# Kernel tuning notes

Hardware: AMD Instinct MI355X
Metric: run time of the kernel (lower is better)

Reference implementation:

```python
import jax, jax.numpy as jnp
import numpy as np

N, E = 50000, 800000
IN_DIM, OUT_DIM, EDGE_DIM = 128, 128, 6
LN_EPS = 1e-5


def setup_inputs() -> dict:
    key = jax.random.key(0)
    ks = jax.random.split(key, 9)
    w = lambda k, sh: (jax.random.normal(k, sh, jnp.float32) * 0.05)
    return {
        "x": jax.random.normal(ks[0], (N, IN_DIM), jnp.float32),
        "edge_attr": jax.random.normal(ks[1], (E, EDGE_DIM), jnp.float32),
        "Wn": w(ks[2], (IN_DIM, OUT_DIM)),
        "bn": jnp.zeros((OUT_DIM,), jnp.float32),
        "We": w(ks[3], (EDGE_DIM, OUT_DIM)),
        "be": jnp.zeros((OUT_DIM,), jnp.float32),
        "Wm": w(ks[4], (2 * OUT_DIM, OUT_DIM)),
        "bm": jnp.zeros((OUT_DIM,), jnp.float32),
        "gamma": jnp.ones((OUT_DIM,), jnp.float32),
        "beta": jnp.zeros((OUT_DIM,), jnp.float32),
        "edge_index": jax.random.randint(ks[5], (2, E), 0, N, jnp.int32),
    }


def reference(x, edge_attr, Wn, bn, We, be, Wm, bm, gamma, beta, edge_index):
    row, col = edge_index[0], edge_index[1]
    x_t = x @ Wn + bn                                  # [N, D]
    e_t = edge_attr @ We + be                          # [E, D]
    msgs = jnp.concatenate([x_t[col], e_t], axis=-1)   # gather + concat [E, 2D]
    msgs = jax.nn.relu(msgs @ Wm + bm)                 # [E, D]
    agg = jax.ops.segment_sum(msgs, row, num_segments=N)            # scatter_add
    deg = jax.ops.segment_sum(jnp.ones((E,), jnp.float32), row, num_segments=N)
    out = agg / jnp.clip(deg, 1.0)[:, None] + x_t      # mean-normalize + residual
    mu = out.mean(axis=-1, keepdims=True)
    var = out.var(axis=-1, keepdims=True)
    return (out - mu) * jax.lax.rsqrt(var + LN_EPS) * gamma + beta
```

## Files before the change

kernel.cpp:

```cpp
#include <hip/hip_runtime.h>
#include <hip/hip_bf16.h>

#define D 128
#define EDGE_DIM 6
#define LN_EPS 1e-5f
#define HIST_BLOCKS 2048

typedef __attribute__((ext_vector_type(8))) short short8;
typedef __attribute__((ext_vector_type(4))) float f32x4;

static __device__ __forceinline__ float bf_lo(unsigned u) { return __uint_as_float(u << 16); }
static __device__ __forceinline__ float bf_hi(unsigned u) { return __uint_as_float(u & 0xffff0000u); }
static __device__ __forceinline__ unsigned short f2bf(float f) {
    __hip_bfloat16 h = __float2bfloat16(f);
    return *reinterpret_cast<unsigned short*>(&h);
}

__global__ __launch_bounds__(128)
void setup_all(const float* __restrict__ Wn, const float* __restrict__ bn,
               const float* __restrict__ We, const float* __restrict__ be,
               const float* __restrict__ Wm, const float* __restrict__ bm,
               const int* __restrict__ ei, int E,
               float* __restrict__ Wnm, float* __restrict__ bnm,
               float* __restrict__ Wc, float* __restrict__ bc,
               int* __restrict__ cnt) {
    const int b = blockIdx.x;
    const int d = threadIdx.x;
    if (b < 128) {
        float acc = 0.f;
#pragma unroll 8
        for (int j = 0; j < D; ++j)
            acc = fmaf(Wn[b * D + j], Wm[j * D + d], acc);
        Wnm[b * D + d] = acc;
    } else if (b == 128) {
        float acc = 0.f;
#pragma unroll 8
        for (int j = 0; j < D; ++j)
            acc = fmaf(bn[j], Wm[j * D + d], acc);
        bnm[d] = acc;
    } else if (b < 135) {
        const int k = b - 129;
        float acc = 0.f;
#pragma unroll 8
        for (int j = 0; j < D; ++j)
            acc = fmaf(We[k * D + j], Wm[(D + j) * D + d], acc);
        Wc[k * D + d] = acc;
    } else if (b == 135) {
        float acc = bm[d];
#pragma unroll 8
        for (int j = 0; j < D; ++j)
            acc = fmaf(be[j], Wm[(D + j) * D + d], acc);
        bc[d] = acc;
    } else {
        for (int i = (b - 136) * 128 + d; i < E; i += HIST_BLOCKS * 128)
            atomicAdd(&cnt[ei[i]], 1);
    }
}

__global__ __launch_bounds__(256)
void pack_wb(const float* __restrict__ Wn, const float* __restrict__ Wnm,
             unsigned short* __restrict__ Wb) {
    const int idx = blockIdx.x * 256 + threadIdx.x;
    if (idx >= 4096) return;
    const int lane = idx & 63;
    const int s = (idx >> 6) & 3;
    const int ct = (idx >> 8) & 7;
    const int mat = idx >> 11;
    const float* W = mat ? Wnm : Wn;
    const int col = ct * 16 + (lane & 15);
    const int k0 = (lane >> 4) * 8 + 32 * s;
    short8 v;
#pragma unroll
    for (int j = 0; j < 8; ++j)
        v[j] = (short)f2bf(W[(size_t)(k0 + j) * D + col]);
    *reinterpret_cast<short8*>(Wb + (size_t)idx * 8) = v;
}

__global__ __launch_bounds__(256)
void gemm_mfma(const float* __restrict__ x, const unsigned short* __restrict__ Wb,
               const float* __restrict__ bn, const float* __restrict__ bnm,
               unsigned short* __restrict__ xtb, unsigned short* __restrict__ hb,
               int nrows) {
    const int lane = threadIdx.x & 63;
    const int wid = threadIdx.x >> 6;
    const int row16 = lane & 15;
    const int kgrp = lane >> 4;
    const int ntile = (nrows + 15) / 16;

    float biasA[8], biasB[8];
#pragma unroll
    for (int ct = 0; ct < 8; ++ct) {
        biasA[ct] = bn[ct * 16 + row16];
        biasB[ct] = bnm[ct * 16 + row16];
    }

    for (int t = blockIdx.x * 4 + wid; t < ntile; t += gridDim.x * 4) {
        const int ra = t * 16 + row16;
        const bool rv = ra < nrows;
        short8 a[4];
#pragma unroll
        for (int s = 0; s < 4; ++s) {
            const float* xp = x + (size_t)ra * D + kgrp * 8 + 32 * s;
            float4 u0 = rv ? *reinterpret_cast<const float4*>(xp)
                           : make_float4(0.f, 0.f, 0.f, 0.f);
            float4 u1 = rv ? *reinterpret_cast<const float4*>(xp + 4)
                           : make_float4(0.f, 0.f, 0.f, 0.f);
            a[s][0] = (short)f2bf(u0.x); a[s][1] = (short)f2bf(u0.y);
            a[s][2] = (short)f2bf(u0.z); a[s][3] = (short)f2bf(u0.w);
            a[s][4] = (short)f2bf(u1.x); a[s][5] = (short)f2bf(u1.y);
            a[s][6] = (short)f2bf(u1.z); a[s][7] = (short)f2bf(u1.w);
        }
        const int rw0 = t * 16 + kgrp * 4;
#pragma unroll
        for (int mat = 0; mat < 2; ++mat) {
            unsigned short* out = mat ? hb : xtb;
#pragma unroll
            for (int ct = 0; ct < 8; ++ct) {
                f32x4 acc = {0.f, 0.f, 0.f, 0.f};
#pragma unroll
                for (int s = 0; s < 4; ++s) {
                    short8 bfr = *reinterpret_cast<const short8*>(
                        Wb + (size_t)((((mat * 8 + ct) * 4 + s) * 64 + lane)) * 8);
                    acc = __builtin_amdgcn_mfma_f32_16x16x32_bf16(a[s], bfr, acc, 0, 0, 0);
                }
                const float bsc = mat ? biasB[ct] : biasA[ct];
                const int dcol = ct * 16 + row16;
#pragma unroll
                for (int j = 0; j < 4; ++j) {
                    const int r = rw0 + j;
                    if (r < nrows) out[(size_t)r * D + dcol] = f2bf(acc[j] + bsc);
                }
            }
        }
    }
}

__global__ __launch_bounds__(1024)
void scan_block_atomic(const int* __restrict__ cnt, int* __restrict__ start,
                       int* __restrict__ cur, int* __restrict__ cursor, int n) {
    __shared__ int wsum[16];
    __shared__ int sbase;
    const int tid = threadIdx.x, lane = tid & 63, wid = tid >> 6;
    const int i = blockIdx.x * 1024 + tid;
    const int v = (i < n) ? cnt[i] : 0;
    int x = v;
#pragma unroll
    for (int off = 1; off < 64; off <<= 1) {
        int t = __shfl_up(x, off);
        if (lane >= off) x += t;
    }
    if (lane == 63) wsum[wid] = x;
    __syncthreads();
    if (wid == 0) {
        int w = (lane < 16) ? wsum[lane] : 0;
#pragma unroll
        for (int off = 1; off < 16; off <<= 1) {
            int t = __shfl_up(w, off);
            if (lane >= off) w += t;
        }
        if (lane < 16) wsum[lane] = w;
    }
    __syncthreads();
    const int total = wsum[15];
    if (tid == 0) sbase = atomicAdd(cursor, total);
    __syncthreads();
    const int woff = (wid > 0) ? wsum[wid - 1] : 0;
    if (i < n) {
        const int sv = sbase + woff + x - v;
        start[i] = sv;
        cur[i] = sv;
    }
}

__global__ void scatter_rec(const int* __restrict__ ei, int E, const float* __restrict__ ea,
                            int* __restrict__ cur, uint4* __restrict__ rec) {
    int e = blockIdx.x * blockDim.x + threadIdx.x;
    if (e < E) {
        int row = ei[e];
        int col = ei[E + e];
        const float* ep = ea + (size_t)e * EDGE_DIM;
        unsigned b01 = (unsigned)f2bf(ep[0]) | ((unsigned)f2bf(ep[1]) << 16);
        unsigned b23 = (unsigned)f2bf(ep[2]) | ((unsigned)f2bf(ep[3]) << 16);
        unsigned b45 = (unsigned)f2bf(ep[4]) | ((unsigned)f2bf(ep[5]) << 16);
        int pos = atomicAdd(&cur[row], 1);
        rec[pos] = make_uint4((unsigned)col, b01, b23, b45);
    }
}

__global__ __launch_bounds__(256)
void aggregate_ln(const unsigned* __restrict__ h,
                  const int* __restrict__ start, const int* __restrict__ cnt,
                  const uint4* __restrict__ rec,
                  const float* __restrict__ Wc, const float* __restrict__ bc,
                  const unsigned* __restrict__ xtb,
                  const float* __restrict__ gamma, const float* __restrict__ beta,
                  float* __restrict__ out, int nnode) {
    const int lane = threadIdx.x & 63;
    const int wid = threadIdx.x >> 6;

    float2 wc[EDGE_DIM];
#pragma unroll
    for (int k = 0; k < EDGE_DIM; ++k)
        wc[k] = reinterpret_cast<const float2*>(Wc)[k * 64 + lane];
    const float2 bc2 = reinterpret_cast<const float2*>(bc)[lane];
    const float2 g = reinterpret_cast<const float2*>(gamma)[lane];
    const float2 bb = reinterpret_cast<const float2*>(beta)[lane];

    for (int n = blockIdx.x * 4 + wid; n < nnode; n += gridDim.x * 4) {
        const int s = start[n];
        const int c = cnt[n];
        float ax = 0.f, ay = 0.f;
        for (int ibase = 0; ibase < c; ibase += 64) {
            const int m = min(64, c - ibase);
            uint4 rc = make_uint4(0, 0, 0, 0);
            if (lane < m) rc = rec[(size_t)(s + ibase) + lane];
            auto LDH = [&](int j) -> unsigned {
                const int jc = min(j, m - 1);
                const int colj = __builtin_amdgcn_readlane((int)rc.x, jc);
                return h[(unsigned)(colj * 64 + lane)];
            };
            auto COMP = [&](int j, unsigned hv) {
                const unsigned b01 = (unsigned)__builtin_amdgcn_readlane((int)rc.y, j);
                const unsigned b23 = (unsigned)__builtin_amdgcn_readlane((int)rc.z, j);
                const unsigned b45 = (unsigned)__builtin_amdgcn_readlane((int)rc.w, j);
                const float e0 = bf_lo(b01), e1 = bf_hi(b01);
                const float e2 = bf_lo(b23), e3 = bf_hi(b23);
                const float e4 = bf_lo(b45), e5 = bf_hi(b45);
                float vx = bc2.x + bf_lo(hv);
                float vy = bc2.y + bf_hi(hv);
                vx = fmaf(e0, wc[0].x, vx); vy = fmaf(e0, wc[0].y, vy);
                vx = fmaf(e1, wc[1].x, vx); vy = fmaf(e1, wc[1].y, vy);
                vx = fmaf(e2, wc[2].x, vx); vy = fmaf(e2, wc[2].y, vy);
                vx = fmaf(e3, wc[3].x, vx); vy = fmaf(e3, wc[3].y, vy);
                vx = fmaf(e4, wc[4].x, vx); vy = fmaf(e4, wc[4].y, vy);
                vx = fmaf(e5, wc[5].x, vx); vy = fmaf(e5, wc[5].y, vy);
                ax += fmaxf(vx, 0.f);
                ay += fmaxf(vy, 0.f);
            };
            unsigned h0 = LDH(0), h1 = LDH(1), h2 = LDH(2), h3 = LDH(3),
                     h4 = LDH(4), h5 = LDH(5), h6 = LDH(6), h7 = LDH(7);
            int i = 0;
            for (; i + 8 <= m; i += 8) {
                COMP(i + 0, h0); h0 = LDH(i + 8);
                COMP(i + 1, h1); h1 = LDH(i + 9);
                COMP(i + 2, h2); h2 = LDH(i + 10);
                COMP(i + 3, h3); h3 = LDH(i + 11);
                COMP(i + 4, h4); h4 = LDH(i + 12);
                COMP(i + 5, h5); h5 = LDH(i + 13);
                COMP(i + 6, h6); h6 = LDH(i + 14);
                COMP(i + 7, h7); h7 = LDH(i + 15);
            }
            if (i + 0 < m) COMP(i + 0, h0);
            if (i + 1 < m) COMP(i + 1, h1);
            if (i + 2 < m) COMP(i + 2, h2);
            if (i + 3 < m) COMP(i + 3, h3);
            if (i + 4 < m) COMP(i + 4, h4);
            if (i + 5 < m) COMP(i + 5, h5);
            if (i + 6 < m) COMP(i + 6, h6);
        }
        const float inv = 1.0f / fmaxf((float)c, 1.0f);
        const unsigned xu = xtb[(unsigned)(n * 64 + lane)];
        float o0 = fmaf(ax, inv, bf_lo(xu));
        float o1 = fmaf(ay, inv, bf_hi(xu));
        float s1 = o0 + o1, s2 = o0 * o0 + o1 * o1;
#pragma unroll
        for (int off = 32; off; off >>= 1) {
            s1 += __shfl_xor(s1, off);
            s2 += __shfl_xor(s2, off);
        }
        const float mean = s1 * (1.0f / D);
        const float var = s2 * (1.0f / D) - mean * mean;
        const float rstd = rsqrtf(var + LN_EPS);
        float2 r;
        r.x = (o0 - mean) * rstd * g.x + bb.x;
        r.y = (o1 - mean) * rstd * g.y + bb.y;
        reinterpret_cast<float2*>(out)[(size_t)n * 64 + lane] = r;
    }
}

extern "C" void kernel_launch(void* const* d_in, const int* in_sizes, int n_in,
                              void* d_out, int out_size, void* d_ws, size_t ws_size,
                              hipStream_t stream) {
    const float* x     = (const float*)d_in[0];
    const float* eattr = (const float*)d_in[1];
    const float* Wn    = (const float*)d_in[2];
    const float* bn    = (const float*)d_in[3];
    const float* We    = (const float*)d_in[4];
    const float* be    = (const float*)d_in[5];
    const float* Wm    = (const float*)d_in[6];
    const float* bm    = (const float*)d_in[7];
    const float* gamma = (const float*)d_in[8];
    const float* beta  = (const float*)d_in[9];
    const int*   ei    = (const int*)d_in[10];

    const int N = in_sizes[0] / D;
    const int E = in_sizes[10] / 2;

    char* ws = (char*)d_ws;
    unsigned short* xtb = (unsigned short*)ws; ws += (size_t)N * D * 2;
    unsigned short* hb  = (unsigned short*)ws; ws += (size_t)N * D * 2;
    int* ints = (int*)ws;                      ws += (size_t)(N + 4) * 4;
    int* cnt = ints;
    int* cursor = ints + N;
    int* cur    = (int*)ws;                    ws += (size_t)N * 4;
    int* startv = (int*)ws;                    ws += (size_t)N * 4;
    uint4* rec  = (uint4*)ws;                  ws += (size_t)E * 16;
    float* Wnm  = (float*)ws;                  ws += (size_t)D * D * 4;
    float* bnm  = (float*)ws;                  ws += (size_t)D * 4;
    float* Wc   = (float*)ws;                  ws += (size_t)EDGE_DIM * D * 4;
    float* bcv  = (float*)ws;                  ws += (size_t)D * 4;
    unsigned short* Wb = (unsigned short*)ws;  ws += (size_t)2 * 8 * 4 * 64 * 8 * 2;

    hipMemsetAsync(ints, 0, (size_t)(N + 4) * 4, stream);

    setup_all<<<136 + HIST_BLOCKS, 128, 0, stream>>>(Wn, bn, We, be, Wm, bm, ei, E,
                                                     Wnm, bnm, Wc, bcv, cnt);
    pack_wb<<<16, 256, 0, stream>>>(Wn, Wnm, Wb);
    scan_block_atomic<<<(N + 1023) / 1024, 1024, 0, stream>>>(cnt, startv, cur, cursor, N);
    scatter_rec<<<(E + 255) / 256, 256, 0, stream>>>(ei, E, eattr, cur, rec);
    gemm_mfma<<<(((N + 15) / 16) + 3) / 4, 256, 0, stream>>>(x, Wb, bn, bnm, xtb, hb, N);
    aggregate_ln<<<(N + 3) / 4, 256, 0, stream>>>((const unsigned*)hb, startv, cnt, rec,
                                                  Wc, bcv, (const unsigned*)xtb,
                                                  gamma, beta, (float*)d_out, N);
}
```

Before: 182.7 us.

## Fuse weight packing into scan, stage edge attrs in LDS, pack-FMA message math

Merges the weight-packing kernel into the scan kernel as extra blocks, which removes one launch. The scatter kernel now stages edge attributes through shared memory so the global reads are coalesced. The GEMM is relaunched as one 64-thread wave per 16-row tile instead of 4-wave blocks with a grid-stride loop. The aggregation inner loop uses inline v_pk_fma_f32/v_pk_add_f32 asm with scalar edge operands to halve the FMA instruction count. Risks include inline asm constraint correctness (SGPR operands for readlane values) and more, smaller GEMM blocks.

```diff
diff --git a/kernel.cpp b/kernel.cpp
--- a/kernel.cpp
+++ b/kernel.cpp
@@ -8,6 +8,7 @@
 
 typedef __attribute__((ext_vector_type(8))) short short8;
 typedef __attribute__((ext_vector_type(4))) float f32x4;
+typedef __attribute__((ext_vector_type(2))) float f32x2;
 
 static __device__ __forceinline__ float bf_lo(unsigned u) { return __uint_as_float(u << 16); }
 static __device__ __forceinline__ float bf_hi(unsigned u) { return __uint_as_float(u & 0xffff0000u); }
@@ -57,90 +58,33 @@
     }
 }
 
-__global__ __launch_bounds__(256)
-void pack_wb(const float* __restrict__ Wn, const float* __restrict__ Wnm,
-             unsigned short* __restrict__ Wb) {
-    const int idx = blockIdx.x * 256 + threadIdx.x;
-    if (idx >= 4096) return;
-    const int lane = idx & 63;
-    const int s = (idx >> 6) & 3;
-    const int ct = (idx >> 8) & 7;
-    const int mat = idx >> 11;
-    const float* W = mat ? Wnm : Wn;
-    const int col = ct * 16 + (lane & 15);
-    const int k0 = (lane >> 4) * 8 + 32 * s;
-    short8 v;
-#pragma unroll
-    for (int j = 0; j < 8; ++j)
-        v[j] = (short)f2bf(W[(size_t)(k0 + j) * D + col]);
-    *reinterpret_cast<short8*>(Wb + (size_t)idx * 8) = v;
-}
-
-__global__ __launch_bounds__(256)
-void gemm_mfma(const float* __restrict__ x, const unsigned short* __restrict__ Wb,
-               const float* __restrict__ bn, const float* __restrict__ bnm,
-               unsigned short* __restrict__ xtb, unsigned short* __restrict__ hb,
-               int nrows) {
-    const int lane = threadIdx.x & 63;
-    const int wid = threadIdx.x >> 6;
-    const int row16 = lane & 15;
-    const int kgrp = lane >> 4;
-    const int ntile = (nrows + 15) / 16;
-
-    float biasA[8], biasB[8];
-#pragma unroll
-    for (int ct = 0; ct < 8; ++ct) {
-        biasA[ct] = bn[ct * 16 + row16];
-        biasB[ct] = bnm[ct * 16 + row16];
-    }
-
-    for (int t = blockIdx.x * 4 + wid; t < ntile; t += gridDim.x * 4) {
-        const int ra = t * 16 + row16;
-        const bool rv = ra < nrows;
-        short8 a[4];
-#pragma unroll
-        for (int s = 0; s < 4; ++s) {
-            const float* xp = x + (size_t)ra * D + kgrp * 8 + 32 * s;
-            float4 u0 = rv ? *reinterpret_cast<const float4*>(xp)
-                           : make_float4(0.f, 0.f, 0.f, 0.f);
-            float4 u1 = rv ? *reinterpret_cast<const float4*>(xp + 4)
-                           : make_float4(0.f, 0.f, 0.f, 0.f);
-            a[s][0] = (short)f2bf(u0.x); a[s][1] = (short)f2bf(u0.y);
-            a[s][2] = (short)f2bf(u0.z); a[s][3] = (short)f2bf(u0.w);
-            a[s][4] = (short)f2bf(u1.x); a[s][5] = (short)f2bf(u1.y);
-            a[s][6] = (short)f2bf(u1.z); a[s][7] = (short)f2bf(u1.w);
-        }
-        const int rw0 = t * 16 + kgrp * 4;
-#pragma unroll
-        for (int mat = 0; mat < 2; ++mat) {
-            unsigned short* out = mat ? hb : xtb;
-#pragma unroll
-            for (int ct = 0; ct < 8; ++ct) {
-                f32x4 acc = {0.f, 0.f, 0.f, 0.f};
-#pragma unroll
-                for (int s = 0; s < 4; ++s) {
-                    short8 bfr = *reinterpret_cast<const short8*>(
-                        Wb + (size_t)((((mat * 8 + ct) * 4 + s) * 64 + lane)) * 8);
-                    acc = __builtin_amdgcn_mfma_f32_16x16x32_bf16(a[s], bfr, acc, 0, 0, 0);
-                }
-                const float bsc = mat ? biasB[ct] : biasA[ct];
-                const int dcol = ct * 16 + row16;
-#pragma unroll
-                for (int j = 0; j < 4; ++j) {
-                    const int r = rw0 + j;
-                    if (r < nrows) out[(size_t)r * D + dcol] = f2bf(acc[j] + bsc);
-                }
-            }
-        }
-    }
-}
-
 __global__ __launch_bounds__(1024)
-void scan_block_atomic(const int* __restrict__ cnt, int* __restrict__ start,
-                       int* __restrict__ cur, int* __restrict__ cursor, int n) {
+void scan_pack(const int* __restrict__ cnt, int* __restrict__ start,
+               int* __restrict__ cur, int* __restrict__ cursor, int n, int nscan,
+               const float* __restrict__ Wn, const float* __restrict__ Wnm,
+               unsigned short* __restrict__ Wb) {
+    const int tid = threadIdx.x;
+    if ((int)blockIdx.x >= nscan) {
+        const int idx = ((int)blockIdx.x - nscan) * 1024 + tid;
+        if (idx < 4096) {
+            const int lane = idx & 63;
+            const int s = (idx >> 6) & 3;
+            const int ct = (idx >> 8) & 7;
+            const int mat = idx >> 11;
+            const float* W = mat ? Wnm : Wn;
+            const int col = ct * 16 + (lane & 15);
+            const int k0 = (lane >> 4) * 8 + 32 * s;
+            short8 v;
+#pragma unroll
+            for (int j = 0; j < 8; ++j)
+                v[j] = (short)f2bf(W[(size_t)(k0 + j) * D + col]);
+            *reinterpret_cast<short8*>(Wb + (size_t)idx * 8) = v;
+        }
+        return;
+    }
     __shared__ int wsum[16];
     __shared__ int sbase;
-    const int tid = threadIdx.x, lane = tid & 63, wid = tid >> 6;
+    const int lane = tid & 63, wid = tid >> 6;
     const int i = blockIdx.x * 1024 + tid;
     const int v = (i < n) ? cnt[i] : 0;
     int x = v;
@@ -172,18 +116,86 @@
     }
 }
 
-__global__ void scatter_rec(const int* __restrict__ ei, int E, const float* __restrict__ ea,
-                            int* __restrict__ cur, uint4* __restrict__ rec) {
-    int e = blockIdx.x * blockDim.x + threadIdx.x;
+__global__ __launch_bounds__(256)
+void scatter_rec(const int* __restrict__ ei, int E, const float* __restrict__ ea,
+                 int* __restrict__ cur, uint4* __restrict__ rec) {
+    __shared__ float sEA[256 * EDGE_DIM];
+    const int tid = threadIdx.x;
+    const int base = blockIdx.x * 256;
+    const size_t gbase = (size_t)base * EDGE_DIM;
+    const size_t gtot = (size_t)E * EDGE_DIM;
+#pragma unroll
+    for (int k = 0; k < EDGE_DIM; ++k) {
+        const int idx = k * 256 + tid;
+        if (gbase + idx < gtot) sEA[idx] = ea[gbase + idx];
+    }
+    __syncthreads();
+    const int e = base + tid;
     if (e < E) {
-        int row = ei[e];
-        int col = ei[E + e];
-        const float* ep = ea + (size_t)e * EDGE_DIM;
+        const int row = ei[e];
+        const int col = ei[E + e];
+        const float* ep = &sEA[tid * EDGE_DIM];
         unsigned b01 = (unsigned)f2bf(ep[0]) | ((unsigned)f2bf(ep[1]) << 16);
         unsigned b23 = (unsigned)f2bf(ep[2]) | ((unsigned)f2bf(ep[3]) << 16);
         unsigned b45 = (unsigned)f2bf(ep[4]) | ((unsigned)f2bf(ep[5]) << 16);
         int pos = atomicAdd(&cur[row], 1);
         rec[pos] = make_uint4((unsigned)col, b01, b23, b45);
+    }
+}
+
+__global__ __launch_bounds__(64)
+void gemm_mfma(const float* __restrict__ x, const unsigned short* __restrict__ Wb,
+               const float* __restrict__ bn, const float* __restrict__ bnm,
+               unsigned short* __restrict__ xtb, unsigned short* __restrict__ hb,
+               int nrows) {
+    const int lane = threadIdx.x;
+    const int row16 = lane & 15;
+    const int kgrp = lane >> 4;
+    const int t = blockIdx.x;
+
+    float biasA[8], biasB[8];
+#pragma unroll
+    for (int ct = 0; ct < 8; ++ct) {
+        biasA[ct] = bn[ct * 16 + row16];
+        biasB[ct] = bnm[ct * 16 + row16];
+    }
+
+    const int ra = t * 16 + row16;
+    const bool rv = ra < nrows;
+    short8 a[4];
+#pragma unroll
+    for (int s = 0; s < 4; ++s) {
+        const float* xp = x + (size_t)ra * D + kgrp * 8 + 32 * s;
+        float4 u0 = rv ? *reinterpret_cast<const float4*>(xp)
+                       : make_float4(0.f, 0.f, 0.f, 0.f);
+        float4 u1 = rv ? *reinterpret_cast<const float4*>(xp + 4)
+                       : make_float4(0.f, 0.f, 0.f, 0.f);
+        a[s][0] = (short)f2bf(u0.x); a[s][1] = (short)f2bf(u0.y);
+        a[s][2] = (short)f2bf(u0.z); a[s][3] = (short)f2bf(u0.w);
+        a[s][4] = (short)f2bf(u1.x); a[s][5] = (short)f2bf(u1.y);
+        a[s][6] = (short)f2bf(u1.z); a[s][7] = (short)f2bf(u1.w);
+    }
+    const int rw0 = t * 16 + kgrp * 4;
+#pragma unroll
+    for (int mat = 0; mat < 2; ++mat) {
+        unsigned short* out = mat ? hb : xtb;
+#pragma unroll
+        for (int ct = 0; ct < 8; ++ct) {
+            f32x4 acc = {0.f, 0.f, 0.f, 0.f};
+#pragma unroll
+            for (int s = 0; s < 4; ++s) {
+                short8 bfr = *reinterpret_cast<const short8*>(
+                    Wb + (size_t)((((mat * 8 + ct) * 4 + s) * 64 + lane)) * 8);
+                acc = __builtin_amdgcn_mfma_f32_16x16x32_bf16(a[s], bfr, acc, 0, 0, 0);
+            }
+            const float bsc = mat ? biasB[ct] : biasA[ct];
+            const int dcol = ct * 16 + row16;
+#pragma unroll
+            for (int j = 0; j < 4; ++j) {
+                const int r = rw0 + j;
+                if (r < nrows) out[(size_t)r * D + dcol] = f2bf(acc[j] + bsc);
+            }
+        }
     }
 }
 
@@ -198,18 +210,18 @@
     const int lane = threadIdx.x & 63;
     const int wid = threadIdx.x >> 6;
 
-    float2 wc[EDGE_DIM];
+    f32x2 wc[EDGE_DIM];
 #pragma unroll
     for (int k = 0; k < EDGE_DIM; ++k)
-        wc[k] = reinterpret_cast<const float2*>(Wc)[k * 64 + lane];
-    const float2 bc2 = reinterpret_cast<const float2*>(bc)[lane];
-    const float2 g = reinterpret_cast<const float2*>(gamma)[lane];
-    const float2 bb = reinterpret_cast<const float2*>(beta)[lane];
+        wc[k] = reinterpret_cast<const f32x2*>(Wc)[k * 64 + lane];
+    const f32x2 bc2 = reinterpret_cast<const f32x2*>(bc)[lane];
+    const f32x2 g = reinterpret_cast<const f32x2*>(gamma)[lane];
+    const f32x2 bb = reinterpret_cast<const f32x2*>(beta)[lane];
 
     for (int n = blockIdx.x * 4 + wid; n < nnode; n += gridDim.x * 4) {
         const int s = start[n];
         const int c = cnt[n];
-        float ax = 0.f, ay = 0.f;
+        f32x2 axy = {0.f, 0.f};
         for (int ibase = 0; ibase < c; ibase += 64) {
             const int m = min(64, c - ibase);
             uint4 rc = make_uint4(0, 0, 0, 0);
@@ -223,19 +235,26 @@
                 const unsigned b01 = (unsigned)__builtin_amdgcn_readlane((int)rc.y, j);
                 const unsigned b23 = (unsigned)__builtin_amdgcn_readlane((int)rc.z, j);
                 const unsigned b45 = (unsigned)__builtin_amdgcn_readlane((int)rc.w, j);
-                const float e0 = bf_lo(b01), e1 = bf_hi(b01);
-                const float e2 = bf_lo(b23), e3 = bf_hi(b23);
-                const float e4 = bf_lo(b45), e5 = bf_hi(b45);
-                float vx = bc2.x + bf_lo(hv);
-                float vy = bc2.y + bf_hi(hv);
-                vx = fmaf(e0, wc[0].x, vx); vy = fmaf(e0, wc[0].y, vy);
-                vx = fmaf(e1, wc[1].x, vx); vy = fmaf(e1, wc[1].y, vy);
-                vx = fmaf(e2, wc[2].x, vx); vy = fmaf(e2, wc[2].y, vy);
-                vx = fmaf(e3, wc[3].x, vx); vy = fmaf(e3, wc[3].y, vy);
-                vx = fmaf(e4, wc[4].x, vx); vy = fmaf(e4, wc[4].y, vy);
-                vx = fmaf(e5, wc[5].x, vx); vy = fmaf(e5, wc[5].y, vy);
-                ax += fmaxf(vx, 0.f);
-                ay += fmaxf(vy, 0.f);
+                f32x2 e01, e23, e45, hx, msg;
+                e01[0] = bf_lo(b01); e01[1] = bf_hi(b01);
+                e23[0] = bf_lo(b23); e23[1] = bf_hi(b23);
+                e45[0] = bf_lo(b45); e45[1] = bf_hi(b45);
+                hx[0] = bf_lo(hv); hx[1] = bf_hi(hv);
+                asm("v_pk_add_f32 %0, %1, %2" : "=v"(msg) : "v"(bc2), "v"(hx));
+                asm("v_pk_fma_f32 %0, %1, %2, %0 op_sel:[0,0,0] op_sel_hi:[0,1,1]"
+                    : "+v"(msg) : "s"(e01), "v"(wc[0]));
+                asm("v_pk_fma_f32 %0, %1, %2, %0 op_sel:[1,0,0] op_sel_hi:[1,1,1]"
+                    : "+v"(msg) : "s"(e01), "v"(wc[1]));
+                asm("v_pk_fma_f32 %0, %1, %2, %0 op_sel:[0,0,0] op_sel_hi:[0,1,1]"
+                    : "+v"(msg) : "s"(e23), "v"(wc[2]));
+                asm("v_pk_fma_f32 %0, %1, %2, %0 op_sel:[1,0,0] op_sel_hi:[1,1,1]"
+                    : "+v"(msg) : "s"(e23), "v"(wc[3]));
+                asm("v_pk_fma_f32 %0, %1, %2, %0 op_sel:[0,0,0] op_sel_hi:[0,1,1]"
+                    : "+v"(msg) : "s"(e45), "v"(wc[4]));
+                asm("v_pk_fma_f32 %0, %1, %2, %0 op_sel:[1,0,0] op_sel_hi:[1,1,1]"
+                    : "+v"(msg) : "s"(e45), "v"(wc[5]));
+                axy[0] += fmaxf(msg[0], 0.f);
+                axy[1] += fmaxf(msg[1], 0.f);
             };
             unsigned h0 = LDH(0), h1 = LDH(1), h2 = LDH(2), h3 = LDH(3),
                      h4 = LDH(4), h5 = LDH(5), h6 = LDH(6), h7 = LDH(7);
@@ -260,8 +279,8 @@
         }
         const float inv = 1.0f / fmaxf((float)c, 1.0f);
         const unsigned xu = xtb[(unsigned)(n * 64 + lane)];
-        float o0 = fmaf(ax, inv, bf_lo(xu));
-        float o1 = fmaf(ay, inv, bf_hi(xu));
+        float o0 = fmaf(axy[0], inv, bf_lo(xu));
+        float o1 = fmaf(axy[1], inv, bf_hi(xu));
         float s1 = o0 + o1, s2 = o0 * o0 + o1 * o1;
 #pragma unroll
         for (int off = 32; off; off >>= 1) {
@@ -272,8 +291,8 @@
         const float var = s2 * (1.0f / D) - mean * mean;
         const float rstd = rsqrtf(var + LN_EPS);
         float2 r;
-        r.x = (o0 - mean) * rstd * g.x + bb.x;
-        r.y = (o1 - mean) * rstd * g.y + bb.y;
+        r.x = (o0 - mean) * rstd * g[0] + bb[0];
+        r.y = (o1 - mean) * rstd * g[1] + bb[1];
         reinterpret_cast<float2*>(out)[(size_t)n * 64 + lane] = r;
     }
 }
@@ -309,16 +328,19 @@
     float* bnm  = (float*)ws;                  ws += (size_t)D * 4;
     float* Wc   = (float*)ws;                  ws += (size_t)EDGE_DIM * D * 4;
     float* bcv  = (float*)ws;                  ws += (size_t)D * 4;
-    unsigned short* Wb = (unsigned short*)ws;  ws += (size_t)2 * 8 * 4 * 64 * 8 * 2;
+    unsigned short* Wb = (unsigned short*)ws;  ws += (size_t)4096 * 8 * 2;
+
+    const int nscan = (N + 1023) / 1024;
+    const int ntile = (N + 15) / 16;
 
     hipMemsetAsync(ints, 0, (size_t)(N + 4) * 4, stream);
 
     setup_all<<<136 + HIST_BLOCKS, 128, 0, stream>>>(Wn, bn, We, be, Wm, bm, ei, E,
                                                      Wnm, bnm, Wc, bcv, cnt);
-    pack_wb<<<16, 256, 0, stream>>>(Wn, Wnm, Wb);
-    scan_block_atomic<<<(N + 1023) / 1024, 1024, 0, stream>>>(cnt, startv, cur, cursor, N);
+    scan_pack<<<nscan + 4, 1024, 0, stream>>>(cnt, startv, cur, cursor, N, nscan,
+                                              Wn, Wnm, Wb);
     scatter_rec<<<(E + 255) / 256, 256, 0, stream>>>(ei, E, eattr, cur, rec);
-    gemm_mfma<<<(((N + 15) / 16) + 3) / 4, 256, 0, stream>>>(x, Wb, bn, bnm, xtb, hb, N);
+    gemm_mfma<<<ntile, 64, 0, stream>>>(x, Wb, bn, bnm, xtb, hb, N);
     aggregate_ln<<<(N + 3) / 4, 256, 0, stream>>>((const unsigned*)hb, startv, cnt, rec,
                                                   Wc, bcv, (const unsigned*)xtb,
                                                   gamma, beta, (float*)d_out, N);
```

Measured after the change: 178.8 us. -2.1%, faster.
